# Kernel tuning notes

Hardware: AMD Instinct MI355X
Metric: run time of the kernel (lower is better)

Reference implementation:

```python
import jax, jax.numpy as jnp
import numpy as np

B, N, C, H, W = 16, 10, 128, 48, 48

def setup_inputs() -> dict:
    key = jax.random.key(0)
    k0, k1 = jax.random.split(key, 2)
    x = jax.random.normal(k0, (B, N, C, H, W), dtype=jnp.float32)
    # trainable interpolation params, initialized to 0.5 as in the torch module
    pos_dec = jnp.full((N,), 0.5, dtype=jnp.float32)
    length_dec = jnp.full((N,), 0.5, dtype=jnp.float32)
    # 1x1 conv == channel-mixing matmul over N*C channels
    NC = N * C
    conv_w = jax.random.normal(k1, (NC, NC), dtype=jnp.float32) * (1.0 / np.sqrt(NC))
    conv_b = jnp.zeros((NC,), dtype=jnp.float32)
    return {"x": x, "pos_dec": pos_dec, "length_dec": length_dec,
            "conv_w": conv_w, "conv_b": conv_b}


def reference(x, pos_dec, length_dec, conv_w, conv_b):
    b, n, c, h, w = x.shape
    d = c * h * w
    q = x.reshape(b, n, d)          # proj_query (B,N,CHW)
    k = q                           # proj_key has the same flattened features
    # bi_interpolate with pos_int=i, length_int=1 reduces in closed form to:
    #   s0 = (1-pd)*K[i]   + pd*K[i+1]                      (key_short row)
    #   s1 = ld*((1-pd)*K[i+1] + pd*K[i+2])                 (zero-padded short mixed with key_long)
    # where indices wrap mod N (key was concatenated with itself).
    idx = jnp.arange(n)
    k1_ = k[:, (idx + 1) % n]       # (B,N,D)
    k2_ = k[:, (idx + 2) % n]
    pd = pos_dec[None, :, None]
    ld = length_dec[None, :, None]
    s0 = (1.0 - pd) * k + pd * k1_
    s1 = ld * ((1.0 - pd) * k1_ + pd * k2_)
    S = jnp.stack([s0, s1], axis=2)                 # (B,N,2,D) interpolated keys per group
    logits = jnp.einsum('bnd,bnkd->bnk', q, S)      # per-group 2-way attention scores
    attn = jax.nn.softmax(logits, axis=-1)          # softmax over the 2 searched keys
    out = jnp.einsum('bnk,bnkd->bnd', attn, S)      # (B,N,D)
    feat = out.reshape(b, n * c, h, w)
    conv = jnp.einsum('oc,bchw->bohw', conv_w, feat) + conv_b[None, :, None, None]
    return conv + x.reshape(b, n * c, h, w)
```

## Files before the change

kernel.cpp:

```cpp
#include <hip/hip_runtime.h>
#include <hip/hip_bf16.h>

#define BB 16
#define NN 10
#define CC 128
#define HWD 2304
#define DD (CC*HWD)
#define NC (NN*CC)

#define CH2 72
#define CHUNK2 4096

#define BM 128
#define BN 128
#define BK 32
#define TK (NC/BK)

typedef __bf16 bf16x8 __attribute__((ext_vector_type(8)));
typedef float  f32x4  __attribute__((ext_vector_type(4)));

#define FEAT_BYTES ((size_t)BB*HWD*NC*2)
#define WB_BYTES   ((size_t)NC*NC*2)
#define PART_FLOATS (BB*NN*CH2*3)

__device__ __forceinline__ ushort f2bf(float f) {
    __hip_bfloat16 h = __float2bfloat16(f);
    return *reinterpret_cast<ushort*>(&h);
}

__device__ __forceinline__ void gload_lds16(const ushort* g, ushort* l) {
    __builtin_amdgcn_global_load_lds(
        (const __attribute__((address_space(1))) void*)(const void*)g,
        (__attribute__((address_space(3))) void*)(void*)l,
        16, 0, 0);
}

__global__ __launch_bounds__(256) void k_dots(const float* __restrict__ x,
                                              float* __restrict__ part) {
    int blk = blockIdx.x;
    int ch = blk % CH2;
    int b  = blk / CH2;
    const float* base = x + (size_t)b*NN*DD + (size_t)ch*CHUNK2;
    int t = threadIdx.x;

    float4 cur[4], nxt[4], inc[4];
    #pragma unroll
    for (int i = 0; i < 4; ++i) cur[i] = *(const float4*)(base + (size_t)0*DD + i*1024 + t*4);
    #pragma unroll
    for (int i = 0; i < 4; ++i) nxt[i] = *(const float4*)(base + (size_t)1*DD + i*1024 + t*4);

    __shared__ float red[4][3];
    int w = t >> 6, l = t & 63;

    for (int n = 0; n < NN; ++n) {
        int n2 = (n + 2) % NN;
        #pragma unroll
        for (int i = 0; i < 4; ++i) inc[i] = *(const float4*)(base + (size_t)n2*DD + i*1024 + t*4);

        float s0 = 0.f, s1 = 0.f, s2 = 0.f;
        #pragma unroll
        for (int i = 0; i < 4; ++i) {
            s0 += cur[i].x*cur[i].x + cur[i].y*cur[i].y + cur[i].z*cur[i].z + cur[i].w*cur[i].w;
            s1 += cur[i].x*nxt[i].x + cur[i].y*nxt[i].y + cur[i].z*nxt[i].z + cur[i].w*nxt[i].w;
            s2 += cur[i].x*inc[i].x + cur[i].y*inc[i].y + cur[i].z*inc[i].z + cur[i].w*inc[i].w;
        }
        for (int o = 32; o > 0; o >>= 1) {
            s0 += __shfl_down(s0, o);
            s1 += __shfl_down(s1, o);
            s2 += __shfl_down(s2, o);
        }
        if (l == 0) { red[w][0] = s0; red[w][1] = s1; red[w][2] = s2; }
        __syncthreads();
        if (t == 0) {
            float r0 = 0.f, r1 = 0.f, r2 = 0.f;
            #pragma unroll
            for (int i = 0; i < 4; ++i) { r0 += red[i][0]; r1 += red[i][1]; r2 += red[i][2]; }
            float* o = part + ((size_t)(b*NN + n)*CH2 + ch)*3;
            o[0] = r0; o[1] = r1; o[2] = r2;
        }
        __syncthreads();
        #pragma unroll
        for (int i = 0; i < 4; ++i) { cur[i] = nxt[i]; nxt[i] = inc[i]; }
    }
}

__global__ void k_coef(const float* __restrict__ part,
                       const float* __restrict__ pos_dec,
                       const float* __restrict__ len_dec,
                       float* __restrict__ coef) {
    int bn = threadIdx.x;
    if (bn >= BB*NN) return;
    int n = bn % NN;
    float d0 = 0.f, d1 = 0.f, d2 = 0.f;
    const float* p = part + (size_t)bn*CH2*3;
    for (int i = 0; i < CH2; ++i) { d0 += p[i*3]; d1 += p[i*3+1]; d2 += p[i*3+2]; }
    float pd = pos_dec[n], ld = len_dec[n];
    float l0 = (1.f - pd)*d0 + pd*d1;
    float l1 = ld*((1.f - pd)*d1 + pd*d2);
    float m  = fmaxf(l0, l1);
    float e0 = expf(l0 - m), e1 = expf(l1 - m);
    float inv = 1.f/(e0 + e1);
    float a0 = e0*inv, a1 = e1*inv;
    coef[bn*3+0] = a0*(1.f - pd);
    coef[bn*3+1] = a0*pd + a1*ld*(1.f - pd);
    coef[bn*3+2] = a1*ld*pd;
}

__global__ __launch_bounds__(256) void k_wconv(const float* __restrict__ w,
                                               ushort* __restrict__ wb) {
    int i = blockIdx.x*blockDim.x + threadIdx.x;
    size_t idx = (size_t)i*4;
    if (idx >= (size_t)NC*NC) return;
    float4 a = *(const float4*)(w + idx);
    ushort4 o;
    o.x = f2bf(a.x); o.y = f2bf(a.y); o.z = f2bf(a.z); o.w = f2bf(a.w);
    *(ushort4*)(wb + idx) = o;
}

__global__ __launch_bounds__(256) void k_feat(const float* __restrict__ x,
                                              const float* __restrict__ coef,
                                              ushort* __restrict__ featT) {
    __shared__ float tile[32*129];
    int hwt = blockIdx.x;
    int b   = blockIdx.y;
    int t = threadIdx.x;
    int hw0 = hwt*32;
    const float* xb = x + (size_t)b*NN*DD;

    int c_[4], ch_[4];
    size_t off_[4];
    #pragma unroll
    for (int i = 0; i < 4; ++i) {
        int s = i*256 + t;
        c_[i] = s >> 3; ch_[i] = s & 7;
        off_[i] = (size_t)c_[i]*HWD + hw0 + ch_[i]*4;
    }

    float4 s0[4], s1[4], s2[4], s3[4];
    #pragma unroll
    for (int i = 0; i < 4; ++i) s0[i] = *(const float4*)(xb + (size_t)0*DD + off_[i]);
    #pragma unroll
    for (int i = 0; i < 4; ++i) s1[i] = *(const float4*)(xb + (size_t)1*DD + off_[i]);
    #pragma unroll
    for (int i = 0; i < 4; ++i) s2[i] = *(const float4*)(xb + (size_t)2*DD + off_[i]);

    for (int n = 0; n < NN; ++n) {
        int n3 = (n + 3) % NN;
        #pragma unroll
        for (int i = 0; i < 4; ++i) s3[i] = *(const float4*)(xb + (size_t)n3*DD + off_[i]);

        int bn = b*NN + n;
        float c0 = coef[bn*3+0], c1 = coef[bn*3+1], c2 = coef[bn*3+2];

        #pragma unroll
        for (int i = 0; i < 4; ++i) {
            int hwb = ch_[i]*4, cc = c_[i];
            tile[(hwb+0)*129 + cc] = c0*s0[i].x + c1*s1[i].x + c2*s2[i].x;
            tile[(hwb+1)*129 + cc] = c0*s0[i].y + c1*s1[i].y + c2*s2[i].y;
            tile[(hwb+2)*129 + cc] = c0*s0[i].z + c1*s1[i].z + c2*s2[i].z;
            tile[(hwb+3)*129 + cc] = c0*s0[i].w + c1*s1[i].w + c2*s2[i].w;
        }
        __syncthreads();

        int hwl = t >> 4;
        int cc0 = (t & 15) * 8;
        #pragma unroll
        for (int p = 0; p < 2; ++p) {
            int hw = p*16 + hwl;
            const float* src = &tile[hw*129 + cc0];
            union { ushort us[8]; uint4 v; } pk;
            #pragma unroll
            for (int j = 0; j < 8; ++j) pk.us[j] = f2bf(src[j]);
            ushort* dst = featT + (size_t)b*HWD*NC + (size_t)(hw0 + hw)*NC + n*CC + cc0;
            *(uint4*)dst = pk.v;
        }
        __syncthreads();
        #pragma unroll
        for (int i = 0; i < 4; ++i) { s0[i] = s1[i]; s1[i] = s2[i]; s2[i] = s3[i]; }
    }
}

__global__ __launch_bounds__(256, 4) void k_gemm(const ushort* __restrict__ Wb,
                                                 const ushort* __restrict__ featT,
                                                 const float* __restrict__ bias,
                                                 const float* __restrict__ x,
                                                 float* __restrict__ out) {
    __shared__ ushort As[2][BM*BK];
    __shared__ ushort Bs[2][BN*BK];

    int bid = blockIdx.x;
    int wkid = (bid & 7) * 360 + (bid >> 3);
    int b    = wkid / 180;
    int rem  = wkid % 180;
    int hwt  = rem / 10;
    int ot   = rem % 10;
    int o0 = ot*BM, hw0 = hwt*BN;

    int t = threadIdx.x;
    int l = t & 63;
    int w = t >> 6;
    int wr = w >> 1, wc = w & 1;

    const ushort* Ag = Wb + (size_t)o0*NC;
    const ushort* Bg = featT + (size_t)b*HWD*NC + (size_t)hw0*NC;

    int r0 = t >> 2, c0 = t & 3;
    size_t g0 = (size_t)r0*NC + (size_t)((c0 ^ ((r0 >> 1) & 3)) * 8);
    size_t g1 = g0 + (size_t)64*NC;

#define STAGE(buf_, kt_) do { \
    size_t k0_ = (size_t)(kt_)*BK; \
    ushort* da_ = &As[buf_][0]; \
    ushort* db_ = &Bs[buf_][0]; \
    gload_lds16(Ag + g0 + k0_, da_ + t*8); \
    gload_lds16(Ag + g1 + k0_, da_ + (256 + t)*8); \
    gload_lds16(Bg + g0 + k0_, db_ + t*8); \
    gload_lds16(Bg + g1 + k0_, db_ + (256 + t)*8); \
} while (0)

    int fr = l & 15;
    int fc = l >> 4;

    f32x4 acc[4][4] = {};

    STAGE(0, 0);
    __syncthreads();

    for (int kt = 0; kt < TK; ++kt) {
        int buf = kt & 1;
        if (kt + 1 < TK) STAGE(buf ^ 1, kt + 1);
        __builtin_amdgcn_sched_barrier(0);

        const ushort* as = &As[buf][0];
        const ushort* bs = &Bs[buf][0];

        bf16x8 afr[4], bfr[4];
        #pragma unroll
        for (int m = 0; m < 4; ++m) {
            int row = wr*64 + m*16 + fr;
            afr[m] = *(const bf16x8*)&as[row*BK + ((fc ^ ((row >> 1) & 3))*8)];
        }
        #pragma unroll
        for (int n = 0; n < 4; ++n) {
            int row = wc*64 + n*16 + fr;
            bfr[n] = *(const bf16x8*)&bs[row*BK + ((fc ^ ((row >> 1) & 3))*8)];
        }
        #pragma unroll
        for (int m = 0; m < 4; ++m)
            #pragma unroll
            for (int n = 0; n < 4; ++n)
                acc[m][n] = __builtin_amdgcn_mfma_f32_16x16x32_bf16(afr[m], bfr[n], acc[m][n], 0, 0, 0);

        __syncthreads();
    }
#undef STAGE

    #pragma unroll
    for (int m = 0; m < 4; ++m) {
        int ro_base = o0 + wr*64 + m*16 + ((l >> 4) << 2);
        #pragma unroll
        for (int n = 0; n < 4; ++n) {
            int col = hw0 + wc*64 + n*16 + (l & 15);
            #pragma unroll
            for (int r = 0; r < 4; ++r) {
                int ro = ro_base + r;
                size_t idx = (size_t)b*NC*HWD + (size_t)ro*HWD + col;
                out[idx] = acc[m][n][r] + bias[ro] + x[idx];
            }
        }
    }
}

extern "C" void kernel_launch(void* const* d_in, const int* in_sizes, int n_in,
                              void* d_out, int out_size, void* d_ws, size_t ws_size,
                              hipStream_t stream) {
    const float* x       = (const float*)d_in[0];
    const float* pos_dec = (const float*)d_in[1];
    const float* len_dec = (const float*)d_in[2];
    const float* conv_w  = (const float*)d_in[3];
    const float* conv_b  = (const float*)d_in[4];
    float* out = (float*)d_out;

    char* ws = (char*)d_ws;
    ushort* featT = (ushort*)ws;
    ushort* wb    = (ushort*)(ws + FEAT_BYTES);
    float*  part  = (float*)(ws + FEAT_BYTES + WB_BYTES);
    float*  coef  = part + PART_FLOATS;

    k_dots <<<dim3(BB*CH2), 256, 0, stream>>>(x, part);
    k_coef <<<dim3(1), 256, 0, stream>>>(part, pos_dec, len_dec, coef);
    k_wconv<<<dim3(1600), 256, 0, stream>>>(conv_w, wb);
    k_feat <<<dim3(72, BB), 256, 0, stream>>>(x, coef, featT);
    k_gemm <<<dim3(2880), 256, 0, stream>>>(wb, featT, conv_b, x, out);
}
```

Measured before the change: 314.5 us.

## Load GEMM MFMA fragments directly from global memory, drop LDS staging

Replaces the LDS double-buffered tiles in the GEMM with per-wave fragment loads straight from global memory into registers, double-buffered in registers across k-steps. This removes the __syncthreads barriers and the LDS writes and reads, but each wave now fetches its own A and B fragments, so there is no intra-block reuse through shared memory. Global traffic goes up and more registers are held, so the launch bound drops to 3 blocks per CU. The change relies on L2/L1 caching to absorb the duplicated loads.

```diff
diff --git a/kernel.cpp b/kernel.cpp
--- a/kernel.cpp
+++ b/kernel.cpp
@@ -26,13 +26,6 @@
 __device__ __forceinline__ ushort f2bf(float f) {
     __hip_bfloat16 h = __float2bfloat16(f);
     return *reinterpret_cast<ushort*>(&h);
-}
-
-__device__ __forceinline__ void gload_lds16(const ushort* g, ushort* l) {
-    __builtin_amdgcn_global_load_lds(
-        (const __attribute__((address_space(1))) void*)(const void*)g,
-        (__attribute__((address_space(3))) void*)(void*)l,
-        16, 0, 0);
 }
 
 __global__ __launch_bounds__(256) void k_dots(const float* __restrict__ x,
@@ -180,14 +173,11 @@
     }
 }
 
-__global__ __launch_bounds__(256, 4) void k_gemm(const ushort* __restrict__ Wb,
+__global__ __launch_bounds__(256, 3) void k_gemm(const ushort* __restrict__ Wb,
                                                  const ushort* __restrict__ featT,
                                                  const float* __restrict__ bias,
                                                  const float* __restrict__ x,
                                                  float* __restrict__ out) {
-    __shared__ ushort As[2][BM*BK];
-    __shared__ ushort Bs[2][BN*BK];
-
     int bid = blockIdx.x;
     int wkid = (bid & 7) * 360 + (bid >> 3);
     int b    = wkid / 180;
@@ -201,59 +191,44 @@
     int w = t >> 6;
     int wr = w >> 1, wc = w & 1;
 
-    const ushort* Ag = Wb + (size_t)o0*NC;
-    const ushort* Bg = featT + (size_t)b*HWD*NC + (size_t)hw0*NC;
-
-    int r0 = t >> 2, c0 = t & 3;
-    size_t g0 = (size_t)r0*NC + (size_t)((c0 ^ ((r0 >> 1) & 3)) * 8);
-    size_t g1 = g0 + (size_t)64*NC;
-
-#define STAGE(buf_, kt_) do { \
-    size_t k0_ = (size_t)(kt_)*BK; \
-    ushort* da_ = &As[buf_][0]; \
-    ushort* db_ = &Bs[buf_][0]; \
-    gload_lds16(Ag + g0 + k0_, da_ + t*8); \
-    gload_lds16(Ag + g1 + k0_, da_ + (256 + t)*8); \
-    gload_lds16(Bg + g0 + k0_, db_ + t*8); \
-    gload_lds16(Bg + g1 + k0_, db_ + (256 + t)*8); \
+    int fr = l & 15;
+    int kc = (l >> 4) * 8;
+
+    const ushort* Abase = Wb    + (size_t)(o0 + wr*64 + fr)*NC + kc;
+    const ushort* Bbase = featT + (size_t)b*HWD*NC + (size_t)(hw0 + wc*64 + fr)*NC + kc;
+
+    f32x4 acc[4][4] = {};
+    bf16x8 a0[4], b0[4], a1[4], b1[4];
+
+#define LOADF(af_, bf_, kt_) do { \
+    size_t ko_ = (size_t)(kt_)*BK; \
+    _Pragma("unroll") \
+    for (int m = 0; m < 4; ++m) af_[m] = *(const bf16x8*)(Abase + (size_t)m*16*NC + ko_); \
+    _Pragma("unroll") \
+    for (int n = 0; n < 4; ++n) bf_[n] = *(const bf16x8*)(Bbase + (size_t)n*16*NC + ko_); \
 } while (0)
 
-    int fr = l & 15;
-    int fc = l >> 4;
-
-    f32x4 acc[4][4] = {};
-
-    STAGE(0, 0);
-    __syncthreads();
-
-    for (int kt = 0; kt < TK; ++kt) {
-        int buf = kt & 1;
-        if (kt + 1 < TK) STAGE(buf ^ 1, kt + 1);
-        __builtin_amdgcn_sched_barrier(0);
-
-        const ushort* as = &As[buf][0];
-        const ushort* bs = &Bs[buf][0];
-
-        bf16x8 afr[4], bfr[4];
-        #pragma unroll
-        for (int m = 0; m < 4; ++m) {
-            int row = wr*64 + m*16 + fr;
-            afr[m] = *(const bf16x8*)&as[row*BK + ((fc ^ ((row >> 1) & 3))*8)];
-        }
-        #pragma unroll
-        for (int n = 0; n < 4; ++n) {
-            int row = wc*64 + n*16 + fr;
-            bfr[n] = *(const bf16x8*)&bs[row*BK + ((fc ^ ((row >> 1) & 3))*8)];
-        }
-        #pragma unroll
-        for (int m = 0; m < 4; ++m)
-            #pragma unroll
-            for (int n = 0; n < 4; ++n)
-                acc[m][n] = __builtin_amdgcn_mfma_f32_16x16x32_bf16(afr[m], bfr[n], acc[m][n], 0, 0, 0);
-
-        __syncthreads();
-    }
-#undef STAGE
+#define MFMA16(af_, bf_) do { \
+    _Pragma("unroll") \
+    for (int m = 0; m < 4; ++m) \
+        _Pragma("unroll") \
+        for (int n = 0; n < 4; ++n) \
+            acc[m][n] = __builtin_amdgcn_mfma_f32_16x16x32_bf16(af_[m], bf_[n], acc[m][n], 0, 0, 0); \
+} while (0)
+
+    LOADF(a0, b0, 0);
+    for (int kt = 0; kt + 2 < TK; kt += 2) {
+        LOADF(a1, b1, kt + 1);
+        MFMA16(a0, b0);
+        LOADF(a0, b0, kt + 2);
+        MFMA16(a1, b1);
+    }
+    LOADF(a1, b1, TK - 1);
+    MFMA16(a0, b0);
+    MFMA16(a1, b1);
+
+#undef LOADF
+#undef MFMA16
 
     #pragma unroll
     for (int m = 0; m < 4; ++m) {
```

Result: slower. 597.3 us (+89.9%).
